# Optimization experiments

Measured on AMD Instinct MI355X. Metric: run time of the kernel, lower is better.

Reference implementation:

```python
import jax, jax.numpy as jnp
import numpy as np
from math import sqrt

EPS_LN = 1e-5

def _layernorm(x, g, b):
    m = x.mean(-1, keepdims=True)
    v = x.var(-1, keepdims=True)
    return (x - m) / jnp.sqrt(v + EPS_LN) * g + b

def _prob_attn(q, k, v, samp, u):
    # Informer ProbSparse self-attention (single head). q,k,v: [B,L,D], samp: [L,U] sampled key ids.
    B, L, D = q.shape
    k_s = k[:, samp]                                   # [B,L,U,D] sampled keys per query
    qk = jnp.einsum('bld,blud->blu', q, k_s)           # [B,L,U]
    M = qk.max(-1) - qk.mean(-1)                       # sparsity measure [B,L]
    _, top = jax.lax.top_k(M, u)                       # [B,u] active queries
    q_r = jnp.take_along_axis(q, top[..., None], axis=1)         # [B,u,D]
    attn = jax.nn.softmax(jnp.einsum('bud,bld->bul', q_r, k) / sqrt(D), axis=-1)
    upd = jnp.einsum('bul,bld->bud', attn, v)                    # [B,u,D]
    ctx = jnp.broadcast_to(v.mean(axis=1, keepdims=True), (B, L, D))  # lazy queries get mean(V)
    return ctx.at[jnp.arange(B)[:, None], top].set(upd)

def _block(x, p, samp, u):
    # ProbSparse attention block: attn + add&norm + FFN + add&norm
    qw, qb, kw, kb, vw, vb, ow, ob, g1, b1, f1w, f1b, f2w, f2b, g2, b2 = p
    q = x @ qw + qb; k = x @ kw + kb; v = x @ vw + vb
    a = _prob_attn(q, k, v, samp, u) @ ow + ob
    x = _layernorm(x + a, g1, b1)
    ff = jnp.maximum(x @ f1w + f1b, 0.0) @ f2w + f2b
    return _layernorm(x + ff, g2, b2)

def _softpool(x, w1, b1, w2, b2):
    # learned soft-pooling: MLP score per position, softmax over window of 2, weighted sum
    B, L, D = x.shape
    s = jnp.maximum(x @ w1 + b1, 0.0) @ w2 + b2        # [B,L]
    w = jax.nn.softmax(s.reshape(B, L // 2, 2), axis=-1)
    return jnp.einsum('blk,blkd->bld', w, x.reshape(B, L // 2, 2, D))

def _forward(x, pe_w, pe_b, qw, qb, kw, kb, vw, vb, ow, ob, ln1g, ln1b,
             f1w, f1b, f2w, f2b, ln2g, ln2b,
             sp1w1, sp1b1, sp1w2, sp1b2, sp2w1, sp2b1, sp2w2, sp2b2,
             dr_w, dr_b, fc1w, fc1b, fc2w, fc2b, fow, fob,
             samp1, samp2, samp3):
    B, N = x.shape
    normed = x / (x.max() - x.min() + 1e-6)
    h = jnp.stack([x, normed], axis=-1)                # [B,N,2]
    h = h.reshape(B, N // 2, 2, 2).mean(axis=2)        # AvgPool1d(2,2) over length -> [B,148,2]
    L = N // 2
    pos = jnp.arange(L, dtype=h.dtype)
    pe = jnp.stack([jnp.sin(pos), jnp.cos(pos)], axis=-1)  # positionalencoding1d(2, L)
    h = jnp.concatenate([h, jnp.broadcast_to(pe, (B, L, 2))], axis=-1)  # [B,148,4]
    h = h @ pe_w + pe_b                                # [B,148,8]
    us = (25, 25, 20)                                  # factor=5, u = 5*ceil(ln(L))
    samps = (samp1, samp2, samp3)
    for i in range(3):
        p = (qw[i], qb[i], kw[i], kb[i], vw[i], vb[i], ow[i], ob[i],
             ln1g[i], ln1b[i], f1w[i], f1b[i], f2w[i], f2b[i], ln2g[i], ln2b[i])
        h = _block(h, p, samps[i], us[i])
        if i == 0:
            h = _softpool(h, sp1w1, sp1b1, sp1w2, sp1b2)   # 148 -> 74
        if i == 1:
            h = _softpool(h, sp2w1, sp2b1, sp2w2, sp2b2)   # 74 -> 37
    h = h @ dr_w + dr_b                                # Conv1d(8,4,1) == pointwise linear -> [B,37,4]
    h = h.reshape(B, -1)                               # [B,148]
    h = jnp.maximum(h @ fc1w + fc1b, 0.0)
    h = jnp.maximum(h @ fc2w + fc2b, 0.0)
    return jax.nn.sigmoid(h @ fow + fob)               # [B,1]


def setup_inputs() -> dict:
    key = jax.random.key(0)
    ks = iter(jax.random.split(key, 64))
    def n(shape, s=0.1):
        return jax.random.normal(next(ks), shape, jnp.float32) * s
    B, N = 4096, 296
    inp = {}
    inp['x'] = jax.random.normal(next(ks), (B, N), jnp.float32)
    inp['samp1'] = jax.random.randint(next(ks), (148, 25), 0, 148)
    inp['samp2'] = jax.random.randint(next(ks), (74, 25), 0, 74)
    inp['samp3'] = jax.random.randint(next(ks), (37, 20), 0, 37)
    inp['pe_w'], inp['pe_b'] = n((4, 8)), n((8,))
    for name, shape in [('qw', (3, 8, 8)), ('qb', (3, 8)), ('kw', (3, 8, 8)), ('kb', (3, 8)),
                        ('vw', (3, 8, 8)), ('vb', (3, 8)), ('ow', (3, 8, 8)), ('ob', (3, 8)),
                        ('f1w', (3, 8, 12)), ('f1b', (3, 12)), ('f2w', (3, 12, 8)), ('f2b', (3, 8))]:
        inp[name] = n(shape)
    inp['ln1g'] = jnp.ones((3, 8), jnp.float32); inp['ln1b'] = jnp.zeros((3, 8), jnp.float32)
    inp['ln2g'] = jnp.ones((3, 8), jnp.float32); inp['ln2b'] = jnp.zeros((3, 8), jnp.float32)
    for pfx in ('sp1', 'sp2'):
        inp[pfx + 'w1'] = n((8, 12)); inp[pfx + 'b1'] = n((12,))
        inp[pfx + 'w2'] = n((12,));   inp[pfx + 'b2'] = n(())
    inp['dr_w'], inp['dr_b'] = n((8, 4)), n((4,))
    inp['fc1w'], inp['fc1b'] = n((148, 74)), n((74,))
    inp['fc2w'], inp['fc2b'] = n((74, 37)), n((37,))
    inp['fow'], inp['fob'] = n((37, 1)), n((1,))
    return inp


def reference(x, samp1, samp2, samp3, pe_w, pe_b, qw, qb, kw, kb, vw, vb, ow, ob,
              ln1g, ln1b, f1w, f1b, f2w, f2b, ln2g, ln2b,
              sp1w1, sp1b1, sp1w2, sp1b2, sp2w1, sp2b1, sp2w2, sp2b2,
              dr_w, dr_b, fc1w, fc1b, fc2w, fc2b, fow, fob):
    return _forward(x, pe_w, pe_b, qw, qb, kw, kb, vw, vb, ow, ob, ln1g, ln1b,
                    f1w, f1b, f2w, f2b, ln2g, ln2b,
                    sp1w1, sp1b1, sp1w2, sp1b2, sp2w1, sp2b1, sp2w2, sp2b2,
                    dr_w, dr_b, fc1w, fc1b, fc2w, fc2b, fow, fob,
                    samp1, samp2, samp3)
```

## Files before the change

### kernel.cpp

```cpp
#include <hip/hip_runtime.h>
#include <math.h>

#define NTHR 256

struct Params {
    const float* x;
    const int*   samp1;
    const int*   samp2;
    const int*   samp3;
    const float* pe_w; const float* pe_b;
    const float* qw; const float* qb;
    const float* kw; const float* kb;
    const float* vw; const float* vb;
    const float* ow; const float* ob;
    const float* f1w; const float* f1b;
    const float* f2w; const float* f2b;
    const float* ln1g; const float* ln1b;
    const float* ln2g; const float* ln2b;
    const float* sp1w1; const float* sp1b1; const float* sp1w2; const float* sp1b2;
    const float* sp2w1; const float* sp2b1; const float* sp2w2; const float* sp2b2;
    const float* dr_w; const float* dr_b;
    const float* fc1w; const float* fc1b;
    const float* fc2w; const float* fc2b;
    const float* fow;  const float* fob;
    const float* scale;
    float* out;
};

__global__ __launch_bounds__(256) void minmax_part(const float4* __restrict__ x4, int n4,
                                                   float* __restrict__ part) {
    float mx = -INFINITY, mn = INFINITY;
    for (int i = blockIdx.x * blockDim.x + threadIdx.x; i < n4; i += gridDim.x * blockDim.x) {
        float4 v = x4[i];
        mx = fmaxf(fmaxf(fmaxf(mx, v.x), fmaxf(v.y, v.z)), v.w);
        mn = fminf(fminf(fminf(mn, v.x), fminf(v.y, v.z)), v.w);
    }
#pragma unroll
    for (int o = 32; o; o >>= 1) {
        mx = fmaxf(mx, __shfl_xor(mx, o));
        mn = fminf(mn, __shfl_xor(mn, o));
    }
    __shared__ float smx[4], smn[4];
    if ((threadIdx.x & 63) == 0) { smx[threadIdx.x >> 6] = mx; smn[threadIdx.x >> 6] = mn; }
    __syncthreads();
    if (threadIdx.x == 0) {
        for (int w = 1; w < 4; ++w) { mx = fmaxf(mx, smx[w]); mn = fminf(mn, smn[w]); }
        part[blockIdx.x * 2]     = mx;
        part[blockIdx.x * 2 + 1] = mn;
    }
}

__global__ __launch_bounds__(256) void minmax_final(const float* __restrict__ part, int nb,
                                                    float* __restrict__ scale) {
    float mx = -INFINITY, mn = INFINITY;
    for (int i = threadIdx.x; i < nb; i += blockDim.x) {
        mx = fmaxf(mx, part[2 * i]);
        mn = fminf(mn, part[2 * i + 1]);
    }
#pragma unroll
    for (int o = 32; o; o >>= 1) {
        mx = fmaxf(mx, __shfl_xor(mx, o));
        mn = fminf(mn, __shfl_xor(mn, o));
    }
    __shared__ float smx[4], smn[4];
    if ((threadIdx.x & 63) == 0) { smx[threadIdx.x >> 6] = mx; smn[threadIdx.x >> 6] = mn; }
    __syncthreads();
    if (threadIdx.x == 0) {
        for (int w = 1; w < 4; ++w) { mx = fmaxf(mx, smx[w]); mn = fminf(mn, smn[w]); }
        scale[0] = mx - mn + 1e-6f;
    }
}

__global__ __launch_bounds__(256) void fused_forward(Params p) {
    const int b = blockIdx.x;
    const int t = threadIdx.x;

    __shared__ float h [148 * 9];
    __shared__ float qs[148 * 9];
    __shared__ float ks[148 * 9];
    __shared__ float vs[148 * 9];
    __shared__ float sc[25 * 149];
    __shared__ float Mv_unused[4];
    __shared__ float ssp[148];
    __shared__ float headf[148];
    __shared__ float upd[25 * 9];
    __shared__ float smax[25], ssum[25];
    __shared__ float vmean[8];
    __shared__ unsigned long long keys[148];
    __shared__ int   topi[25];
    __shared__ int   sel[148];
    __shared__ int   ntop;
    __shared__ float hd2[37];

    (void)Mv_unused;
    const float dscale = p.scale[0];

    if (t < 148) {
        const float2 xp = ((const float2*)(p.x + b * 296))[t];
        float pin[4];
        pin[0] = 0.5f * (xp.x + xp.y);
        pin[1] = 0.5f * (xp.x / dscale + xp.y / dscale);
        pin[2] = sinf((float)t);
        pin[3] = cosf((float)t);
#pragma unroll
        for (int dd = 0; dd < 8; ++dd) {
            float acc = 0.f;
#pragma unroll
            for (int e = 0; e < 4; ++e) acc += pin[e] * p.pe_w[e * 8 + dd];
            h[t * 9 + dd] = acc + p.pe_b[dd];
        }
    }
    __syncthreads();

    int L = 148;
    for (int layer = 0; layer < 3; ++layer) {
        const float* qw = p.qw + layer * 64;  const float* qb = p.qb + layer * 8;
        const float* kw = p.kw + layer * 64;  const float* kb = p.kb + layer * 8;
        const float* vw = p.vw + layer * 64;  const float* vb = p.vb + layer * 8;
        const float* ow = p.ow + layer * 64;  const float* ob = p.ob + layer * 8;
        const float* f1w = p.f1w + layer * 96; const float* f1b = p.f1b + layer * 12;
        const float* f2w = p.f2w + layer * 96; const float* f2b = p.f2b + layer * 8;
        const float* g1 = p.ln1g + layer * 8; const float* bb1 = p.ln1b + layer * 8;
        const float* g2 = p.ln2g + layer * 8; const float* bb2 = p.ln2b + layer * 8;
        const int* samp = (layer == 0) ? p.samp1 : (layer == 1) ? p.samp2 : p.samp3;
        const int usamp = (layer == 2) ? 20 : 25;
        const int u     = (layer == 2) ? 20 : 25;

        int* samp_s = (int*)sc;
        for (int i = t; i < L * usamp; i += NTHR) samp_s[i] = samp[i];
        if (t == 0) ntop = 0;

        if (t < L) {
            float hr[8];
#pragma unroll
            for (int e = 0; e < 8; ++e) hr[e] = h[t * 9 + e];
#pragma unroll
            for (int dd = 0; dd < 8; ++dd) {
                float aq = 0.f, ak = 0.f, av = 0.f;
#pragma unroll
                for (int e = 0; e < 8; ++e) {
                    aq += hr[e] * qw[e * 8 + dd];
                    ak += hr[e] * kw[e * 8 + dd];
                    av += hr[e] * vw[e * 8 + dd];
                }
                qs[t * 9 + dd] = aq + qb[dd];
                ks[t * 9 + dd] = ak + kb[dd];
                vs[t * 9 + dd] = av + vb[dd];
            }
        }
        __syncthreads();

        if (t < L) {
            float qr[8];
#pragma unroll
            for (int e = 0; e < 8; ++e) qr[e] = qs[t * 9 + e];
            float mx = -INFINITY, sum = 0.f;
            for (int j = 0; j < usamp; ++j) {
                int idx = samp_s[t * usamp + j];
                float acc = 0.f;
#pragma unroll
                for (int e = 0; e < 8; ++e) acc += qr[e] * ks[idx * 9 + e];
                mx = fmaxf(mx, acc);
                sum += acc;
            }
            float M = mx - sum / (float)usamp;
            unsigned ub = __float_as_uint(M);
            ub = (ub & 0x80000000u) ? ~ub : (ub | 0x80000000u);
            keys[t] = ((unsigned long long)ub << 32)
                    | (unsigned long long)(0xFFFFFFFFu - (unsigned)t);
        }
        __syncthreads();

        if (t < L) {
            const unsigned long long mykey = keys[t];
            int rank = 0;
            for (int j = 0; j < L; ++j) rank += (keys[j] > mykey) ? 1 : 0;
            int sj = -1;
            if (rank < u) {
                sj = atomicAdd(&ntop, 1);
                topi[sj] = t;
            }
            sel[t] = sj;
        }
        __syncthreads();

        if (t < L) {
            float kr[8];
#pragma unroll
            for (int e = 0; e < 8; ++e) kr[e] = ks[t * 9 + e];
            for (int j = 0; j < u; ++j) {
                int r = topi[j];
                float acc = 0.f;
#pragma unroll
                for (int e = 0; e < 8; ++e) acc += qs[r * 9 + e] * kr[e];
                sc[j * 149 + t] = acc * 0.35355339059327373f;
            }
        }
        __syncthreads();

        {
            int g = t >> 3, lg = t & 7;
            if (g < u) {
                float mx = -INFINITY;
                for (int l = lg; l < L; l += 8) mx = fmaxf(mx, sc[g * 149 + l]);
#pragma unroll
                for (int o = 4; o; o >>= 1) mx = fmaxf(mx, __shfl_xor(mx, o));
                float sm = 0.f;
                for (int l = lg; l < L; l += 8) sm += __expf(sc[g * 149 + l] - mx);
#pragma unroll
                for (int o = 4; o; o >>= 1) sm += __shfl_xor(sm, o);
                if (lg == 0) { smax[g] = mx; ssum[g] = sm; }
            }
        }
        __syncthreads();

        if (t < L) {
            for (int j = 0; j < u; ++j)
                sc[j * 149 + t] = __expf(sc[j * 149 + t] - smax[j]) / ssum[j];
        }
        if (t >= 248) {
            int dd = t - 248;
            float acc = 0.f;
            for (int l = 0; l < L; ++l) acc += vs[l * 9 + dd];
            vmean[dd] = acc / (float)L;
        }
        __syncthreads();

        if (t < u * 8) {
            int j = t >> 3, dd = t & 7;
            float acc = 0.f;
            for (int l = 0; l < L; ++l) acc += sc[j * 149 + l] * vs[l * 9 + dd];
            upd[j * 9 + dd] = acc;
        }
        __syncthreads();

        if (t < L) {
            float ctx[8];
            int sj = sel[t];
            if (sj >= 0) {
#pragma unroll
                for (int e = 0; e < 8; ++e) ctx[e] = upd[sj * 9 + e];
            } else {
#pragma unroll
                for (int e = 0; e < 8; ++e) ctx[e] = vmean[e];
            }
            float xr[8];
#pragma unroll
            for (int dd = 0; dd < 8; ++dd) {
                float acc = 0.f;
#pragma unroll
                for (int e = 0; e < 8; ++e) acc += ctx[e] * ow[e * 8 + dd];
                xr[dd] = h[t * 9 + dd] + (acc + ob[dd]);
            }
            float mean = 0.f;
#pragma unroll
            for (int e = 0; e < 8; ++e) mean += xr[e];
            mean *= 0.125f;
            float var = 0.f;
#pragma unroll
            for (int e = 0; e < 8; ++e) { float z = xr[e] - mean; var += z * z; }
            var *= 0.125f;
            float inv = 1.0f / sqrtf(var + 1e-5f);
            float y[8];
#pragma unroll
            for (int e = 0; e < 8; ++e) y[e] = (xr[e] - mean) * inv * g1[e] + bb1[e];

            float f1[12];
#pragma unroll
            for (int o = 0; o < 12; ++o) {
                float acc = 0.f;
#pragma unroll
                for (int e = 0; e < 8; ++e) acc += y[e] * f1w[e * 12 + o];
                f1[o] = fmaxf(acc + f1b[o], 0.f);
            }
            float x2[8];
#pragma unroll
            for (int o = 0; o < 8; ++o) {
                float acc = 0.f;
#pragma unroll
                for (int e = 0; e < 12; ++e) acc += f1[e] * f2w[e * 8 + o];
                x2[o] = y[o] + (acc + f2b[o]);
            }
            mean = 0.f;
#pragma unroll
            for (int e = 0; e < 8; ++e) mean += x2[e];
            mean *= 0.125f;
            var = 0.f;
#pragma unroll
            for (int e = 0; e < 8; ++e) { float z = x2[e] - mean; var += z * z; }
            var *= 0.125f;
            inv = 1.0f / sqrtf(var + 1e-5f);
#pragma unroll
            for (int e = 0; e < 8; ++e) h[t * 9 + e] = (x2[e] - mean) * inv * g2[e] + bb2[e];
        }
        __syncthreads();

        if (layer < 2) {
            const float* w1  = layer ? p.sp2w1 : p.sp1w1;
            const float* sb1 = layer ? p.sp2b1 : p.sp1b1;
            const float* w2  = layer ? p.sp2w2 : p.sp1w2;
            const float* sb2 = layer ? p.sp2b2 : p.sp1b2;
            if (t < L) {
                float yr[8];
#pragma unroll
                for (int e = 0; e < 8; ++e) yr[e] = h[t * 9 + e];
                float acc2 = 0.f;
#pragma unroll
                for (int o = 0; o < 12; ++o) {
                    float acc = 0.f;
#pragma unroll
                    for (int e = 0; e < 8; ++e) acc += yr[e] * w1[e * 12 + o];
                    acc2 += fmaxf(acc + sb1[o], 0.f) * w2[o];
                }
                ssp[t] = acc2 + sb2[0];
            }
            __syncthreads();
            int Lh = L >> 1;
            float nrow[8];
            if (t < Lh) {
                float s0 = ssp[2 * t], s1 = ssp[2 * t + 1];
                float m = fmaxf(s0, s1);
                float e0 = __expf(s0 - m), e1 = __expf(s1 - m);
                float den = e0 + e1;
                float w0 = e0 / den, w1v = e1 / den;
#pragma unroll
                for (int e = 0; e < 8; ++e)
                    nrow[e] = w0 * h[(2 * t) * 9 + e] + w1v * h[(2 * t + 1) * 9 + e];
            }
            __syncthreads();
            if (t < Lh) {
#pragma unroll
                for (int e = 0; e < 8; ++e) h[t * 9 + e] = nrow[e];
            }
            __syncthreads();
            L = Lh;
        }
    }

    if (t < 37) {
        float yr[8];
#pragma unroll
        for (int e = 0; e < 8; ++e) yr[e] = h[t * 9 + e];
#pragma unroll
        for (int c = 0; c < 4; ++c) {
            float acc = 0.f;
#pragma unroll
            for (int e = 0; e < 8; ++e) acc += yr[e] * p.dr_w[e * 4 + c];
            headf[t * 4 + c] = acc + p.dr_b[c];
        }
    }
    __syncthreads();
    if (t < 74) {
        float acc = 0.f;
        for (int i = 0; i < 148; ++i) acc += headf[i] * p.fc1w[i * 74 + t];
        ssp[t] = fmaxf(acc + p.fc1b[t], 0.f);
    }
    __syncthreads();
    if (t < 37) {
        float acc = 0.f;
        for (int i = 0; i < 74; ++i) acc += ssp[i] * p.fc2w[i * 37 + t];
        hd2[t] = fmaxf(acc + p.fc2b[t], 0.f);
    }
    __syncthreads();
    if (t == 0) {
        float acc = 0.f;
        for (int i = 0; i < 37; ++i) acc += hd2[i] * p.fow[i];
        acc += p.fob[0];
        p.out[b] = 1.f / (1.f + __expf(-acc));
    }
}

extern "C" void kernel_launch(void* const* d_in, const int* in_sizes, int n_in,
                              void* d_out, int out_size, void* d_ws, size_t ws_size,
                              hipStream_t stream) {
    Params p;
    p.x     = (const float*)d_in[0];
    p.samp1 = (const int*)d_in[1];
    p.samp2 = (const int*)d_in[2];
    p.samp3 = (const int*)d_in[3];
    p.pe_w  = (const float*)d_in[4];  p.pe_b  = (const float*)d_in[5];
    p.qw    = (const float*)d_in[6];  p.qb    = (const float*)d_in[7];
    p.kw    = (const float*)d_in[8];  p.kb    = (const float*)d_in[9];
    p.vw    = (const float*)d_in[10]; p.vb    = (const float*)d_in[11];
    p.ow    = (const float*)d_in[12]; p.ob    = (const float*)d_in[13];
    p.f1w   = (const float*)d_in[14]; p.f1b   = (const float*)d_in[15];
    p.f2w   = (const float*)d_in[16]; p.f2b   = (const float*)d_in[17];
    p.ln1g  = (const float*)d_in[18]; p.ln1b  = (const float*)d_in[19];
    p.ln2g  = (const float*)d_in[20]; p.ln2b  = (const float*)d_in[21];
    p.sp1w1 = (const float*)d_in[22]; p.sp1b1 = (const float*)d_in[23];
    p.sp1w2 = (const float*)d_in[24]; p.sp1b2 = (const float*)d_in[25];
    p.sp2w1 = (const float*)d_in[26]; p.sp2b1 = (const float*)d_in[27];
    p.sp2w2 = (const float*)d_in[28]; p.sp2b2 = (const float*)d_in[29];
    p.dr_w  = (const float*)d_in[30]; p.dr_b  = (const float*)d_in[31];
    p.fc1w  = (const float*)d_in[32]; p.fc1b  = (const float*)d_in[33];
    p.fc2w  = (const float*)d_in[34]; p.fc2b  = (const float*)d_in[35];
    p.fow   = (const float*)d_in[36]; p.fob   = (const float*)d_in[37];

    const int n = in_sizes[0];
    const int B = n / 296;

    float* wsf   = (float*)d_ws;
    float* part  = wsf;
    float* scale = wsf + 512;

    minmax_part<<<256, 256, 0, stream>>>((const float4*)p.x, n / 4, part);
    minmax_final<<<1, 256, 0, stream>>>(part, 256, scale);

    p.scale = scale;
    p.out   = (float*)d_out;
    fused_forward<<<B, 256, 0, stream>>>(p);
}
```

Baseline: 391.6 us.

## Template layers, shrink shared memory, fold minmax final into main kernel

Each layer is now a template specialised on L, sample count and u, so loops become compile-time and unrollable. Shared memory drops sharply: the q buffer, the top-index and selection arrays, and the sample staging copy are removed; the selected queries are kept in registers and copied to a small buffer; attention scores are processed in chunks of 13 queries in a reused region. This raises occupancy, and launch_bounds now asks for 6 blocks per CU. The separate minmax_final launch is removed and every block reduces the 256 partials itself, saving one launch at the cost of redundant per-block work and more barriers from the chunked softmax.

```diff
diff --git a/kernel.cpp b/kernel.cpp
--- a/kernel.cpp
+++ b/kernel.cpp
@@ -23,7 +23,7 @@
     const float* fc1w; const float* fc1b;
     const float* fc2w; const float* fc2b;
     const float* fow;  const float* fob;
-    const float* scale;
+    const float* part;
     float* out;
 };
 
@@ -50,50 +50,272 @@
     }
 }
 
-__global__ __launch_bounds__(256) void minmax_final(const float* __restrict__ part, int nb,
-                                                    float* __restrict__ scale) {
-    float mx = -INFINITY, mn = INFINITY;
-    for (int i = threadIdx.x; i < nb; i += blockDim.x) {
-        mx = fmaxf(mx, part[2 * i]);
-        mn = fminf(mn, part[2 * i + 1]);
-    }
-#pragma unroll
-    for (int o = 32; o; o >>= 1) {
-        mx = fmaxf(mx, __shfl_xor(mx, o));
-        mn = fminf(mn, __shfl_xor(mn, o));
-    }
-    __shared__ float smx[4], smn[4];
-    if ((threadIdx.x & 63) == 0) { smx[threadIdx.x >> 6] = mx; smn[threadIdx.x >> 6] = mn; }
-    __syncthreads();
-    if (threadIdx.x == 0) {
-        for (int w = 1; w < 4; ++w) { mx = fmaxf(mx, smx[w]); mn = fminf(mn, smn[w]); }
-        scale[0] = mx - mn + 1e-6f;
+template<int L, int USAMP, int U, bool POOL>
+__device__ __forceinline__ void layer_fn(
+    const int t,
+    float* __restrict__ h, float* __restrict__ ks, float* __restrict__ vs,
+    float* __restrict__ region, float* __restrict__ q_sel, float* __restrict__ upd,
+    float* __restrict__ smax, float* __restrict__ ssum, float* __restrict__ vmean,
+    int* __restrict__ ntop,
+    const float* qw, const float* qb, const float* kw, const float* kb,
+    const float* vw, const float* vb, const float* ow, const float* ob,
+    const float* f1w, const float* f1b, const float* f2w, const float* f2b,
+    const float* g1, const float* bb1, const float* g2, const float* bb2,
+    const int* __restrict__ samp,
+    const float* spw1, const float* spb1, const float* spw2, const float* spb2)
+{
+    float* sc = region;
+    unsigned long long* keys = (unsigned long long*)region;
+
+    if (t == 0) *ntop = 0;
+
+    float hr[8], qr[8];
+    if (t < L) {
+#pragma unroll
+        for (int e = 0; e < 8; ++e) hr[e] = h[t * 9 + e];
+#pragma unroll
+        for (int dd = 0; dd < 8; ++dd) {
+            float aq = 0.f, ak = 0.f, av = 0.f;
+#pragma unroll
+            for (int e = 0; e < 8; ++e) {
+                aq += hr[e] * qw[e * 8 + dd];
+                ak += hr[e] * kw[e * 8 + dd];
+                av += hr[e] * vw[e * 8 + dd];
+            }
+            qr[dd] = aq + qb[dd];
+            ks[t * 9 + dd] = ak + kb[dd];
+            vs[t * 9 + dd] = av + vb[dd];
+        }
+    }
+    __syncthreads();
+
+    if (t < L) {
+        const int* srow = samp + t * USAMP;
+        float mx = -INFINITY, sum = 0.f;
+        for (int j = 0; j < USAMP; ++j) {
+            int idx = srow[j];
+            float acc = 0.f;
+#pragma unroll
+            for (int e = 0; e < 8; ++e) acc += qr[e] * ks[idx * 9 + e];
+            mx = fmaxf(mx, acc);
+            sum += acc;
+        }
+        float M = mx - sum / (float)USAMP;
+        unsigned ub = __float_as_uint(M);
+        ub = (ub & 0x80000000u) ? ~ub : (ub | 0x80000000u);
+        keys[t] = ((unsigned long long)ub << 32)
+                | (unsigned long long)(0xFFFFFFFFu - (unsigned)t);
+    }
+    __syncthreads();
+
+    int sj = -1;
+    if (t < L) {
+        const unsigned long long mykey = keys[t];
+        int rank = 0;
+#pragma unroll 16
+        for (int j = 0; j < L; ++j) rank += (keys[j] > mykey) ? 1 : 0;
+        if (rank < U) {
+            sj = atomicAdd(ntop, 1);
+#pragma unroll
+            for (int e = 0; e < 8; ++e) q_sel[sj * 9 + e] = qr[e];
+        }
+    }
+    __syncthreads();
+
+#pragma unroll
+    for (int c0 = 0; c0 < U; c0 += 13) {
+        const int cn = (U - c0) < 13 ? (U - c0) : 13;
+
+        if (t < L) {
+            float kr[8];
+#pragma unroll
+            for (int e = 0; e < 8; ++e) kr[e] = ks[t * 9 + e];
+#pragma unroll
+            for (int j = 0; j < cn; ++j) {
+                float acc = 0.f;
+#pragma unroll
+                for (int e = 0; e < 8; ++e) acc += q_sel[(c0 + j) * 9 + e] * kr[e];
+                sc[j * 149 + t] = acc * 0.35355339059327373f;
+            }
+        }
+        if (c0 == 0 && t >= 248) {
+            int dd = t - 248;
+            float acc = 0.f;
+#pragma unroll 4
+            for (int l = 0; l < L; ++l) acc += vs[l * 9 + dd];
+            vmean[dd] = acc / (float)L;
+        }
+        __syncthreads();
+
+        {
+            int g = t >> 3, lg = t & 7;
+            if (g < cn) {
+                float mx = -INFINITY;
+                for (int l = lg; l < L; l += 8) mx = fmaxf(mx, sc[g * 149 + l]);
+#pragma unroll
+                for (int o = 4; o; o >>= 1) mx = fmaxf(mx, __shfl_xor(mx, o));
+                float sm = 0.f;
+                for (int l = lg; l < L; l += 8) sm += __expf(sc[g * 149 + l] - mx);
+#pragma unroll
+                for (int o = 4; o; o >>= 1) sm += __shfl_xor(sm, o);
+                if (lg == 0) { smax[g] = mx; ssum[g] = sm; }
+            }
+        }
+        __syncthreads();
+
+        if (t < L) {
+#pragma unroll
+            for (int j = 0; j < cn; ++j)
+                sc[j * 149 + t] = __expf(sc[j * 149 + t] - smax[j]) / ssum[j];
+        }
+        __syncthreads();
+
+        if (t < cn * 8) {
+            int j = t >> 3, dd = t & 7;
+            float a0 = 0.f, a1 = 0.f;
+#pragma unroll 8
+            for (int l = 0; l < (L & ~1); l += 2) {
+                a0 += sc[j * 149 + l]     * vs[l * 9 + dd];
+                a1 += sc[j * 149 + l + 1] * vs[(l + 1) * 9 + dd];
+            }
+            float a = a0 + a1;
+            if (L & 1) a += sc[j * 149 + (L - 1)] * vs[(L - 1) * 9 + dd];
+            upd[(c0 + j) * 9 + dd] = a;
+        }
+        __syncthreads();
+    }
+
+    if (t < L) {
+        float ctx[8];
+        if (sj >= 0) {
+#pragma unroll
+            for (int e = 0; e < 8; ++e) ctx[e] = upd[sj * 9 + e];
+        } else {
+#pragma unroll
+            for (int e = 0; e < 8; ++e) ctx[e] = vmean[e];
+        }
+        float xr[8];
+#pragma unroll
+        for (int dd = 0; dd < 8; ++dd) {
+            float acc = 0.f;
+#pragma unroll
+            for (int e = 0; e < 8; ++e) acc += ctx[e] * ow[e * 8 + dd];
+            xr[dd] = hr[dd] + (acc + ob[dd]);
+        }
+        float mean = 0.f;
+#pragma unroll
+        for (int e = 0; e < 8; ++e) mean += xr[e];
+        mean *= 0.125f;
+        float var = 0.f;
+#pragma unroll
+        for (int e = 0; e < 8; ++e) { float z = xr[e] - mean; var += z * z; }
+        var *= 0.125f;
+        float inv = 1.0f / sqrtf(var + 1e-5f);
+        float y[8];
+#pragma unroll
+        for (int e = 0; e < 8; ++e) y[e] = (xr[e] - mean) * inv * g1[e] + bb1[e];
+
+        float f1[12];
+#pragma unroll
+        for (int o = 0; o < 12; ++o) {
+            float acc = 0.f;
+#pragma unroll
+            for (int e = 0; e < 8; ++e) acc += y[e] * f1w[e * 12 + o];
+            f1[o] = fmaxf(acc + f1b[o], 0.f);
+        }
+        float x2[8];
+#pragma unroll
+        for (int o = 0; o < 8; ++o) {
+            float acc = 0.f;
+#pragma unroll
+            for (int e = 0; e < 12; ++e) acc += f1[e] * f2w[e * 8 + o];
+            x2[o] = y[o] + (acc + f2b[o]);
+        }
+        mean = 0.f;
+#pragma unroll
+        for (int e = 0; e < 8; ++e) mean += x2[e];
+        mean *= 0.125f;
+        var = 0.f;
+#pragma unroll
+        for (int e = 0; e < 8; ++e) { float z = x2[e] - mean; var += z * z; }
+        var *= 0.125f;
+        inv = 1.0f / sqrtf(var + 1e-5f);
+        float y2[8];
+#pragma unroll
+        for (int e = 0; e < 8; ++e) {
+            y2[e] = (x2[e] - mean) * inv * g2[e] + bb2[e];
+            h[t * 9 + e] = y2[e];
+        }
+
+        if (POOL) {
+            float acc2 = 0.f;
+#pragma unroll
+            for (int o = 0; o < 12; ++o) {
+                float acc = 0.f;
+#pragma unroll
+                for (int e = 0; e < 8; ++e) acc += y2[e] * spw1[e * 12 + o];
+                acc2 += fmaxf(acc + spb1[o], 0.f) * spw2[o];
+            }
+            region[t] = acc2 + spb2[0];
+        }
+    }
+    __syncthreads();
+
+    if (POOL) {
+        constexpr int Lh = L / 2;
+        float nrow[8];
+        float w0 = 0.f, w1v = 0.f;
+        if (t < Lh) {
+            float s0 = region[2 * t], s1 = region[2 * t + 1];
+            float m = fmaxf(s0, s1);
+            float e0 = __expf(s0 - m), e1 = __expf(s1 - m);
+            float den = e0 + e1;
+            w0 = e0 / den; w1v = e1 / den;
+#pragma unroll
+            for (int e = 0; e < 8; ++e)
+                nrow[e] = w0 * h[(2 * t) * 9 + e] + w1v * h[(2 * t + 1) * 9 + e];
+        }
+        __syncthreads();
+        if (t < Lh) {
+#pragma unroll
+            for (int e = 0; e < 8; ++e) h[t * 9 + e] = nrow[e];
+        }
+        __syncthreads();
     }
 }
 
-__global__ __launch_bounds__(256) void fused_forward(Params p) {
+__global__ __launch_bounds__(256, 6) void fused_forward(Params p) {
     const int b = blockIdx.x;
     const int t = threadIdx.x;
 
     __shared__ float h [148 * 9];
-    __shared__ float qs[148 * 9];
     __shared__ float ks[148 * 9];
     __shared__ float vs[148 * 9];
-    __shared__ float sc[25 * 149];
-    __shared__ float Mv_unused[4];
-    __shared__ float ssp[148];
-    __shared__ float headf[148];
+    __shared__ __align__(16) float region[13 * 149];
+    __shared__ float q_sel[25 * 9];
     __shared__ float upd[25 * 9];
-    __shared__ float smax[25], ssum[25];
+    __shared__ float smax[13], ssum[13];
     __shared__ float vmean[8];
-    __shared__ unsigned long long keys[148];
-    __shared__ int   topi[25];
-    __shared__ int   sel[148];
     __shared__ int   ntop;
-    __shared__ float hd2[37];
-
-    (void)Mv_unused;
-    const float dscale = p.scale[0];
+    __shared__ float scale_s;
+    __shared__ float smx[4], smn[4];
+
+    {
+        float mx = p.part[2 * t], mn = p.part[2 * t + 1];
+#pragma unroll
+        for (int o = 32; o; o >>= 1) {
+            mx = fmaxf(mx, __shfl_xor(mx, o));
+            mn = fminf(mn, __shfl_xor(mn, o));
+        }
+        if ((t & 63) == 0) { smx[t >> 6] = mx; smn[t >> 6] = mn; }
+        __syncthreads();
+        if (t == 0) {
+            for (int w = 1; w < 4; ++w) { mx = fmaxf(mx, smx[w]); mn = fminf(mn, smn[w]); }
+            scale_s = mx - mn + 1e-6f;
+        }
+        __syncthreads();
+    }
+    const float dscale = scale_s;
 
     if (t < 148) {
         const float2 xp = ((const float2*)(p.x + b * 296))[t];
@@ -112,231 +334,25 @@
     }
     __syncthreads();
 
-    int L = 148;
-    for (int layer = 0; layer < 3; ++layer) {
-        const float* qw = p.qw + layer * 64;  const float* qb = p.qb + layer * 8;
-        const float* kw = p.kw + layer * 64;  const float* kb = p.kb + layer * 8;
-        const float* vw = p.vw + layer * 64;  const float* vb = p.vb + layer * 8;
-        const float* ow = p.ow + layer * 64;  const float* ob = p.ob + layer * 8;
-        const float* f1w = p.f1w + layer * 96; const float* f1b = p.f1b + layer * 12;
-        const float* f2w = p.f2w + layer * 96; const float* f2b = p.f2b + layer * 8;
-        const float* g1 = p.ln1g + layer * 8; const float* bb1 = p.ln1b + layer * 8;
-        const float* g2 = p.ln2g + layer * 8; const float* bb2 = p.ln2b + layer * 8;
-        const int* samp = (layer == 0) ? p.samp1 : (layer == 1) ? p.samp2 : p.samp3;
-        const int usamp = (layer == 2) ? 20 : 25;
-        const int u     = (layer == 2) ? 20 : 25;
-
-        int* samp_s = (int*)sc;
-        for (int i = t; i < L * usamp; i += NTHR) samp_s[i] = samp[i];
-        if (t == 0) ntop = 0;
-
-        if (t < L) {
-            float hr[8];
-#pragma unroll
-            for (int e = 0; e < 8; ++e) hr[e] = h[t * 9 + e];
-#pragma unroll
-            for (int dd = 0; dd < 8; ++dd) {
-                float aq = 0.f, ak = 0.f, av = 0.f;
-#pragma unroll
-                for (int e = 0; e < 8; ++e) {
-                    aq += hr[e] * qw[e * 8 + dd];
-                    ak += hr[e] * kw[e * 8 + dd];
-                    av += hr[e] * vw[e * 8 + dd];
-                }
-                qs[t * 9 + dd] = aq + qb[dd];
-                ks[t * 9 + dd] = ak + kb[dd];
-                vs[t * 9 + dd] = av + vb[dd];
-            }
-        }
-        __syncthreads();
-
-        if (t < L) {
-            float qr[8];
-#pragma unroll
-            for (int e = 0; e < 8; ++e) qr[e] = qs[t * 9 + e];
-            float mx = -INFINITY, sum = 0.f;
-            for (int j = 0; j < usamp; ++j) {
-                int idx = samp_s[t * usamp + j];
-                float acc = 0.f;
-#pragma unroll
-                for (int e = 0; e < 8; ++e) acc += qr[e] * ks[idx * 9 + e];
-                mx = fmaxf(mx, acc);
-                sum += acc;
-            }
-            float M = mx - sum / (float)usamp;
-            unsigned ub = __float_as_uint(M);
-            ub = (ub & 0x80000000u) ? ~ub : (ub | 0x80000000u);
-            keys[t] = ((unsigned long long)ub << 32)
-                    | (unsigned long long)(0xFFFFFFFFu - (unsigned)t);
-        }
-        __syncthreads();
-
-        if (t < L) {
-            const unsigned long long mykey = keys[t];
-            int rank = 0;
-            for (int j = 0; j < L; ++j) rank += (keys[j] > mykey) ? 1 : 0;
-            int sj = -1;
-            if (rank < u) {
-                sj = atomicAdd(&ntop, 1);
-                topi[sj] = t;
-            }
-            sel[t] = sj;
-        }
-        __syncthreads();
-
-        if (t < L) {
-            float kr[8];
-#pragma unroll
-            for (int e = 0; e < 8; ++e) kr[e] = ks[t * 9 + e];
-            for (int j = 0; j < u; ++j) {
-                int r = topi[j];
-                float acc = 0.f;
-#pragma unroll
-                for (int e = 0; e < 8; ++e) acc += qs[r * 9 + e] * kr[e];
-                sc[j * 149 + t] = acc * 0.35355339059327373f;
-            }
-        }
-        __syncthreads();
-
-        {
-            int g = t >> 3, lg = t & 7;
-            if (g < u) {
-                float mx = -INFINITY;
-                for (int l = lg; l < L; l += 8) mx = fmaxf(mx, sc[g * 149 + l]);
-#pragma unroll
-                for (int o = 4; o; o >>= 1) mx = fmaxf(mx, __shfl_xor(mx, o));
-                float sm = 0.f;
-                for (int l = lg; l < L; l += 8) sm += __expf(sc[g * 149 + l] - mx);
-#pragma unroll
-                for (int o = 4; o; o >>= 1) sm += __shfl_xor(sm, o);
-                if (lg == 0) { smax[g] = mx; ssum[g] = sm; }
-            }
-        }
-        __syncthreads();
-
-        if (t < L) {
-            for (int j = 0; j < u; ++j)
-                sc[j * 149 + t] = __expf(sc[j * 149 + t] - smax[j]) / ssum[j];
-        }
-        if (t >= 248) {
-            int dd = t - 248;
-            float acc = 0.f;
-            for (int l = 0; l < L; ++l) acc += vs[l * 9 + dd];
-            vmean[dd] = acc / (float)L;
-        }
-        __syncthreads();
-
-        if (t < u * 8) {
-            int j = t >> 3, dd = t & 7;
-            float acc = 0.f;
-            for (int l = 0; l < L; ++l) acc += sc[j * 149 + l] * vs[l * 9 + dd];
-            upd[j * 9 + dd] = acc;
-        }
-        __syncthreads();
-
-        if (t < L) {
-            float ctx[8];
-            int sj = sel[t];
-            if (sj >= 0) {
-#pragma unroll
-                for (int e = 0; e < 8; ++e) ctx[e] = upd[sj * 9 + e];
-            } else {
-#pragma unroll
-                for (int e = 0; e < 8; ++e) ctx[e] = vmean[e];
-            }
-            float xr[8];
-#pragma unroll
-            for (int dd = 0; dd < 8; ++dd) {
-                float acc = 0.f;
-#pragma unroll
-                for (int e = 0; e < 8; ++e) acc += ctx[e] * ow[e * 8 + dd];
-                xr[dd] = h[t * 9 + dd] + (acc + ob[dd]);
-            }
-            float mean = 0.f;
-#pragma unroll
-            for (int e = 0; e < 8; ++e) mean += xr[e];
-            mean *= 0.125f;
-            float var = 0.f;
-#pragma unroll
-            for (int e = 0; e < 8; ++e) { float z = xr[e] - mean; var += z * z; }
-            var *= 0.125f;
-            float inv = 1.0f / sqrtf(var + 1e-5f);
-            float y[8];
-#pragma unroll
-            for (int e = 0; e < 8; ++e) y[e] = (xr[e] - mean) * inv * g1[e] + bb1[e];
-
-            float f1[12];
-#pragma unroll
-            for (int o = 0; o < 12; ++o) {
-                float acc = 0.f;
-#pragma unroll
-                for (int e = 0; e < 8; ++e) acc += y[e] * f1w[e * 12 + o];
-                f1[o] = fmaxf(acc + f1b[o], 0.f);
-            }
-            float x2[8];
-#pragma unroll
-            for (int o = 0; o < 8; ++o) {
-                float acc = 0.f;
-#pragma unroll
-                for (int e = 0; e < 12; ++e) acc += f1[e] * f2w[e * 8 + o];
-                x2[o] = y[o] + (acc + f2b[o]);
-            }
-            mean = 0.f;
-#pragma unroll
-            for (int e = 0; e < 8; ++e) mean += x2[e];
-            mean *= 0.125f;
-            var = 0.f;
-#pragma unroll
-            for (int e = 0; e < 8; ++e) { float z = x2[e] - mean; var += z * z; }
-            var *= 0.125f;
-            inv = 1.0f / sqrtf(var + 1e-5f);
-#pragma unroll
-            for (int e = 0; e < 8; ++e) h[t * 9 + e] = (x2[e] - mean) * inv * g2[e] + bb2[e];
-        }
-        __syncthreads();
-
-        if (layer < 2) {
-            const float* w1  = layer ? p.sp2w1 : p.sp1w1;
-            const float* sb1 = layer ? p.sp2b1 : p.sp1b1;
-            const float* w2  = layer ? p.sp2w2 : p.sp1w2;
-            const float* sb2 = layer ? p.sp2b2 : p.sp1b2;
-            if (t < L) {
-                float yr[8];
-#pragma unroll
-                for (int e = 0; e < 8; ++e) yr[e] = h[t * 9 + e];
-                float acc2 = 0.f;
-#pragma unroll
-                for (int o = 0; o < 12; ++o) {
-                    float acc = 0.f;
-#pragma unroll
-                    for (int e = 0; e < 8; ++e) acc += yr[e] * w1[e * 12 + o];
-                    acc2 += fmaxf(acc + sb1[o], 0.f) * w2[o];
-                }
-                ssp[t] = acc2 + sb2[0];
-            }
-            __syncthreads();
-            int Lh = L >> 1;
-            float nrow[8];
-            if (t < Lh) {
-                float s0 = ssp[2 * t], s1 = ssp[2 * t + 1];
-                float m = fmaxf(s0, s1);
-                float e0 = __expf(s0 - m), e1 = __expf(s1 - m);
-                float den = e0 + e1;
-                float w0 = e0 / den, w1v = e1 / den;
-#pragma unroll
-                for (int e = 0; e < 8; ++e)
-                    nrow[e] = w0 * h[(2 * t) * 9 + e] + w1v * h[(2 * t + 1) * 9 + e];
-            }
-            __syncthreads();
-            if (t < Lh) {
-#pragma unroll
-                for (int e = 0; e < 8; ++e) h[t * 9 + e] = nrow[e];
-            }
-            __syncthreads();
-            L = Lh;
-        }
-    }
-
+    layer_fn<148, 25, 25, true >(t, h, ks, vs, region, q_sel, upd, smax, ssum, vmean, &ntop,
+        p.qw,       p.qb,      p.kw,       p.kb,      p.vw,       p.vb,      p.ow,       p.ob,
+        p.f1w,      p.f1b,     p.f2w,      p.f2b,
+        p.ln1g,     p.ln1b,    p.ln2g,     p.ln2b,    p.samp1,
+        p.sp1w1, p.sp1b1, p.sp1w2, p.sp1b2);
+    layer_fn<74, 25, 25, true >(t, h, ks, vs, region, q_sel, upd, smax, ssum, vmean, &ntop,
+        p.qw + 64,  p.qb + 8,  p.kw + 64,  p.kb + 8,  p.vw + 64,  p.vb + 8,  p.ow + 64,  p.ob + 8,
+        p.f1w + 96, p.f1b + 12, p.f2w + 96, p.f2b + 8,
+        p.ln1g + 8, p.ln1b + 8, p.ln2g + 8, p.ln2b + 8, p.samp2,
+        p.sp2w1, p.sp2b1, p.sp2w2, p.sp2b2);
+    layer_fn<37, 20, 20, false>(t, h, ks, vs, region, q_sel, upd, smax, ssum, vmean, &ntop,
+        p.qw + 128, p.qb + 16, p.kw + 128, p.kb + 16, p.vw + 128, p.vb + 16, p.ow + 128, p.ob + 16,
+        p.f1w + 192, p.f1b + 24, p.f2w + 192, p.f2b + 16,
+        p.ln1g + 16, p.ln1b + 16, p.ln2g + 16, p.ln2b + 16, p.samp3,
+        nullptr, nullptr, nullptr, nullptr);
+
+    float* hf  = region + 256;
+    float* s1b = region;
+    float* hd2 = region + 512;
     if (t < 37) {
         float yr[8];
 #pragma unroll
@@ -346,19 +362,21 @@
             float acc = 0.f;
 #pragma unroll
             for (int e = 0; e < 8; ++e) acc += yr[e] * p.dr_w[e * 4 + c];
-            headf[t * 4 + c] = acc + p.dr_b[c];
+            hf[t * 4 + c] = acc + p.dr_b[c];
         }
     }
     __syncthreads();
     if (t < 74) {
         float acc = 0.f;
-        for (int i = 0; i < 148; ++i) acc += headf[i] * p.fc1w[i * 74 + t];
-        ssp[t] = fmaxf(acc + p.fc1b[t], 0.f);
+#pragma unroll 4
+        for (int i = 0; i < 148; ++i) acc += hf[i] * p.fc1w[i * 74 + t];
+        s1b[t] = fmaxf(acc + p.fc1b[t], 0.f);
     }
     __syncthreads();
     if (t < 37) {
         float acc = 0.f;
-        for (int i = 0; i < 74; ++i) acc += ssp[i] * p.fc2w[i * 37 + t];
+#pragma unroll 2
+        for (int i = 0; i < 74; ++i) acc += s1b[i] * p.fc2w[i * 37 + t];
         hd2[t] = fmaxf(acc + p.fc2b[t], 0.f);
     }
     __syncthreads();
@@ -399,14 +417,11 @@
     const int n = in_sizes[0];
     const int B = n / 296;
 
-    float* wsf   = (float*)d_ws;
-    float* part  = wsf;
-    float* scale = wsf + 512;
+    float* part = (float*)d_ws;
 
     minmax_part<<<256, 256, 0, stream>>>((const float4*)p.x, n / 4, part);
-    minmax_final<<<1, 256, 0, stream>>>(part, 256, scale);
-
-    p.scale = scale;
-    p.out   = (float*)d_out;
+
+    p.part = part;
+    p.out  = (float*)d_out;
     fused_forward<<<B, 256, 0, stream>>>(p);
 }
```

New measurement: 388.0 us. No clear change (-0.9%).
